# Kernel optimization log

Hardware: AMD Instinct MI355X
Metric: run time of the kernel (lower is better)

Reference implementation:

```python
import jax, jax.numpy as jnp
import numpy as np
import math

D_MODEL = 1024
NUM_HEADS = 16
HEAD_DIM = D_MODEL // NUM_HEADS


def setup_inputs() -> dict:
    key = jax.random.key(0)
    ks = jax.random.split(key, 9)
    B, S = 2, 2048
    scale = 1.0 / math.sqrt(D_MODEL)
    x = jax.random.normal(ks[0], (B, S, D_MODEL), dtype=jnp.float32)
    # torch nn.Linear params: weight [out, in], bias [out]
    Wq = jax.random.normal(ks[1], (D_MODEL, D_MODEL), dtype=jnp.float32) * scale
    bq = jax.random.normal(ks[2], (D_MODEL,), dtype=jnp.float32) * scale
    Wk = jax.random.normal(ks[3], (D_MODEL, D_MODEL), dtype=jnp.float32) * scale
    bk = jax.random.normal(ks[4], (D_MODEL,), dtype=jnp.float32) * scale
    Wv = jax.random.normal(ks[5], (D_MODEL, D_MODEL), dtype=jnp.float32) * scale
    bv = jax.random.normal(ks[6], (D_MODEL,), dtype=jnp.float32) * scale
    Wo = jax.random.normal(ks[7], (D_MODEL, D_MODEL), dtype=jnp.float32) * scale
    bo = jax.random.normal(ks[8], (D_MODEL,), dtype=jnp.float32) * scale
    return {"x": x, "Wq": Wq, "bq": bq, "Wk": Wk, "bk": bk,
            "Wv": Wv, "bv": bv, "Wo": Wo, "bo": bo}


def reference(x, Wq, bq, Wk, bk, Wv, bv, Wo, bo):
    B, S, _ = x.shape
    H, Dh = NUM_HEADS, HEAD_DIM

    def proj(W, b):
        # torch Linear: x @ W.T + b -> [B,S,D] -> [B,H,S,Dh]
        y = jnp.einsum('bsd,ed->bse', x, W) + b
        return y.reshape(B, S, H, Dh).transpose(0, 2, 1, 3)

    Q = proj(Wq, bq)
    K = proj(Wk, bk)
    V = proj(Wv, bv)

    # scores [B,H,S,S], causal mask with -inf, then scale by 1/sqrt(head_dim)
    scores = jnp.einsum('bhqd,bhkd->bhqk', Q, K)
    causal = jnp.tril(jnp.ones((S, S), dtype=bool))
    scores = jnp.where(causal, scores, -jnp.inf)
    A = jax.nn.softmax(scores / math.sqrt(Dh), axis=-1)

    O = jnp.einsum('bhqk,bhkd->bhqd', A, V)  # [B,H,S,Dh]
    O = O.transpose(0, 2, 1, 3).reshape(B, S, H * Dh)
    return jnp.einsum('bsd,ed->bse', O, Wo) + bo
```

## Files before the change

### kernel.cpp

```cpp
#include <hip/hip_runtime.h>


typedef _Float16 f16x8 __attribute__((ext_vector_type(8)));
typedef _Float16 f16x4 __attribute__((ext_vector_type(4)));
typedef _Float16 f16x2 __attribute__((ext_vector_type(2)));
typedef float f32x4 __attribute__((ext_vector_type(4)));

#define S_  2048
#define DM  1024
#define NH  16
#define DH  64

__device__ __forceinline__ void gload_lds16(const void* g, void* s) {
  __builtin_amdgcn_global_load_lds(
      (const __attribute__((address_space(1))) void*)g,
      (__attribute__((address_space(3))) void*)s, 16, 0, 0);
}

__device__ __forceinline__ f16x2 pkrtz(float a, float b) {
  return __builtin_bit_cast(f16x2, __builtin_amdgcn_cvt_pkrtz(a, b));
}


__global__ void cvt_all_kernel(const float* __restrict__ x,
                               const float* __restrict__ w0,
                               const float* __restrict__ w1,
                               const float* __restrict__ w2,
                               const float* __restrict__ w3,
                               _Float16* __restrict__ xb,
                               _Float16* __restrict__ wb) {
  const int bid = blockIdx.x;
  const float* src;
  _Float16* dst;
  int idx;
  if (bid < 4096) {
    src = x; dst = xb; idx = bid * 256 + threadIdx.x;
  } else {
    const int j = bid - 4096;
    const int y = j >> 10;
    src = (y == 0) ? w0 : (y == 1) ? w1 : (y == 2) ? w2 : w3;
    dst = wb + (size_t)y * (DM * DM);
    idx = (j & 1023) * 256 + threadIdx.x;
  }
  const float4 v = ((const float4*)src)[idx];
  f16x4 h;
  h[0] = (_Float16)v.x; h[1] = (_Float16)v.y;
  h[2] = (_Float16)v.z; h[3] = (_Float16)v.w;
  ((f16x4*)dst)[idx] = h;
}


__global__ __launch_bounds__(256, 3) void gemm_qkv_kernel(
    const _Float16* __restrict__ xb, const _Float16* __restrict__ wb,
    const float* __restrict__ bq, const float* __restrict__ bk,
    const float* __restrict__ bv, _Float16* __restrict__ qkv)
{
  __shared__ _Float16 As[2][128 * 32];
  __shared__ _Float16 Ws[2][128 * 32];

  const int i = blockIdx.x;
  const int xcd = i & 7;
  const int tt = i >> 3;
  const int mp = xcd * 4 + (tt & 3);
  const int u = tt >> 2;
  const int np = u & 7;
  const int z = u >> 3;

  const _Float16* W = wb + (size_t)z * (DM * DM);
  const float* bias = (z == 0) ? bq : ((z == 1) ? bk : bv);
  _Float16* out = qkv + (size_t)z * 4194304;

  const f32x4 z4 = {0.f, 0.f, 0.f, 0.f};
  f32x4 acc[4][4];
#pragma unroll
  for (int mi = 0; mi < 4; ++mi)
#pragma unroll
    for (int ni = 0; ni < 4; ++ni) acc[mi][ni] = z4;

  const int m0 = mp * 128, n0 = np * 128;
  const int t = threadIdx.x;
  const int w = t >> 6, l = t & 63;
  const int quad = l >> 4, ln = l & 15;
  const int wm = (w >> 1) << 6, wn = (w & 1) << 6;
  const int srow = l >> 2, scol = (l & 3) << 3;

  for (int k0 = 0; k0 < DM; k0 += 64) {
#pragma unroll
    for (int h = 0; h < 2; ++h)
#pragma unroll
      for (int i2 = 0; i2 < 2; ++i2) {
        const int ra = w * 32 + i2 * 16;
        gload_lds16(&xb[(size_t)(m0 + ra + srow) * DM + k0 + h * 32 + scol],
                    &As[h][ra * 32]);
        gload_lds16(&W[(size_t)(n0 + ra + srow) * DM + k0 + h * 32 + scol],
                    &Ws[h][ra * 32]);
      }
    __syncthreads();

#pragma unroll
    for (int h = 0; h < 2; ++h) {
      f16x8 af[4], bf[4];
#pragma unroll
      for (int mi = 0; mi < 4; ++mi)
        af[mi] = *(const f16x8*)&As[h][(wm + mi * 16 + ln) * 32 + quad * 8];
#pragma unroll
      for (int ni = 0; ni < 4; ++ni)
        bf[ni] = *(const f16x8*)&Ws[h][(wn + ni * 16 + ln) * 32 + quad * 8];
#pragma unroll
      for (int mi = 0; mi < 4; ++mi)
#pragma unroll
        for (int ni = 0; ni < 4; ++ni)
          acc[mi][ni] = __builtin_amdgcn_mfma_f32_16x16x32_f16(
              af[mi], bf[ni], acc[mi][ni], 0, 0, 0);
    }
    __syncthreads();
  }

  const float scale = (z == 0) ? 0.18033688f : 1.0f;

#pragma unroll
  for (int ni = 0; ni < 4; ++ni) {
    const int c = n0 + wn + ni * 16 + ln;
    const float bias_c = bias[c];
    const int h = c >> 6, d = c & 63;
#pragma unroll
    for (int mi = 0; mi < 4; ++mi) {
      const int mb = m0 + wm + mi * 16 + quad * 4;
#pragma unroll
      for (int r = 0; r < 4; ++r) {
        const int mg = mb + r;
        const int b = mg >> 11, s = mg & 2047;
        const int bh = b * NH + h;
        const float v = (acc[mi][ni][r] + bias_c) * scale;
        size_t idx;
        if (z == 2)
          idx = (size_t)bh * 131072 + (s >> 5) * 2048 + (d >> 4) * 512 +
                ((s >> 3) & 3) * 128 + (d & 15) * 8 + (s & 7);
        else
          idx = (size_t)bh * 131072 + (s >> 4) * 1024 + (d >> 5) * 512 +
                ((d >> 3) & 3) * 128 + (s & 15) * 8 + (d & 7);
        out[idx] = (_Float16)v;
      }
    }
  }
}


__global__ __launch_bounds__(256, 2) void gemm_out_kernel(
    const _Float16* __restrict__ ob, const _Float16* __restrict__ wo,
    const float* __restrict__ bo, float* __restrict__ out)
{
  __shared__ _Float16 As[2][128 * 32];
  __shared__ _Float16 Ws[2][64 * 32];

  const int i = blockIdx.x;
  const int xcd = i & 7;
  const int tt = i >> 3;
  const int mp = xcd * 4 + (tt & 3);
  const int np = tt >> 2;

  const f32x4 z4 = {0.f, 0.f, 0.f, 0.f};
  f32x4 acc[2][4];
#pragma unroll
  for (int mi = 0; mi < 2; ++mi)
#pragma unroll
    for (int ni = 0; ni < 4; ++ni) acc[mi][ni] = z4;

  const int m0 = mp * 128, n0 = np * 64;
  const int t = threadIdx.x;
  const int w = t >> 6, l = t & 63;
  const int quad = l >> 4, ln = l & 15;
  const int srow = l >> 2, scol = (l & 3) << 3;

  for (int k0 = 0; k0 < DM; k0 += 64) {
#pragma unroll
    for (int h = 0; h < 2; ++h) {
#pragma unroll
      for (int i2 = 0; i2 < 2; ++i2) {
        const int ra = w * 32 + i2 * 16;
        gload_lds16(&ob[(size_t)(m0 + ra + srow) * DM + k0 + h * 32 + scol],
                    &As[h][ra * 32]);
      }
      gload_lds16(&wo[(size_t)(n0 + w * 16 + srow) * DM + k0 + h * 32 + scol],
                  &Ws[h][w * 16 * 32]);
    }
    __syncthreads();

#pragma unroll
    for (int h = 0; h < 2; ++h) {
      f16x8 af[2], bf[4];
#pragma unroll
      for (int mi = 0; mi < 2; ++mi)
        af[mi] = *(const f16x8*)&As[h][(w * 32 + mi * 16 + ln) * 32 + quad * 8];
#pragma unroll
      for (int ni = 0; ni < 4; ++ni)
        bf[ni] = *(const f16x8*)&Ws[h][(ni * 16 + ln) * 32 + quad * 8];
#pragma unroll
      for (int mi = 0; mi < 2; ++mi)
#pragma unroll
        for (int ni = 0; ni < 4; ++ni)
          acc[mi][ni] = __builtin_amdgcn_mfma_f32_16x16x32_f16(
              af[mi], bf[ni], acc[mi][ni], 0, 0, 0);
    }
    __syncthreads();
  }

#pragma unroll
  for (int ni = 0; ni < 4; ++ni) {
    const int c = n0 + ni * 16 + ln;
    const float bias_c = bo[c];
#pragma unroll
    for (int mi = 0; mi < 2; ++mi) {
      const int mb = m0 + w * 32 + mi * 16 + quad * 4;
#pragma unroll
      for (int r = 0; r < 4; ++r)
        out[(size_t)(mb + r) * DM + c] = acc[mi][ni][r] + bias_c;
    }
  }
}


template <int MODE>
__device__ __forceinline__ void tile64(
    const _Float16* __restrict__ kb_, const _Float16* __restrict__ vb_,
    int t, const f16x8 (&qf)[4][2], f32x4 (&oacc)[4][4], float (&l_i)[4],
    _Float16* Ps, int quad, int ln, int l)
{
  f16x8 kr[4], vr[4];
#pragma unroll
  for (int ii = 0; ii < 4; ++ii)
    kr[ii] = *(const f16x8*)(kb_ + (size_t)t * 2048 + ii * 512 + l * 8);
#pragma unroll
  for (int ii = 0; ii < 4; ++ii)
    vr[ii] = *(const f16x8*)(vb_ + (size_t)t * 2048 + ii * 512 + l * 8);

  const f32x4 z4 = {0.f, 0.f, 0.f, 0.f};
#pragma unroll
  for (int qs = 0; qs < 4; ++qs) {
    if (MODE == 2 && qs < 2) continue;

    f32x4 sacc[2];
    sacc[0] = z4; sacc[1] = z4;
#pragma unroll
    for (int ks = 0; ks < 2; ++ks)
#pragma unroll
      for (int mi = 0; mi < 2; ++mi)
        sacc[mi] = __builtin_amdgcn_mfma_f32_16x16x32_f16(
            kr[mi * 2 + ks], qf[qs][ks], sacc[mi], 0, 0, 0);

    const bool DG = (MODE == 1 && qs < 2) || (MODE == 2);
    const int hq = ((MODE == 1) ? qs : (qs - 2)) << 4;

    float rs = 0.f;
#pragma unroll
    for (int mi = 0; mi < 2; ++mi) {
      float p[4];
#pragma unroll
      for (int r = 0; r < 4; ++r) {
        p[r] = __builtin_amdgcn_exp2f(sacc[mi][r]);
        if (DG && (mi * 16 + quad * 4 + r > hq + ln)) p[r] = 0.f;
        rs += p[r];
      }
      const f16x2 lo = pkrtz(p[0], p[1]);
      const f16x2 hi = pkrtz(p[2], p[3]);
      const f16x4 pk = __builtin_shufflevector(lo, hi, 0, 1, 2, 3);
      const int slot = ((mi * 4 + quad) + 2 * ln) & 15;
      *(f16x4*)&Ps[ln * 64 + slot * 4] = pk;
    }
    l_i[qs] += rs;

    const int slot2 = ((quad * 2) + 2 * ln) & 15;
    const f16x8 pb = *(const f16x8*)&Ps[ln * 64 + slot2 * 4];

#pragma unroll
    for (int di = 0; di < 4; ++di)
      oacc[qs][di] = __builtin_amdgcn_mfma_f32_16x16x32_f16(
          vr[di], pb, oacc[qs][di], 0, 0, 0);
  }
}

__global__ __launch_bounds__(128, 3) void attn_kernel(
    const _Float16* __restrict__ QF, const _Float16* __restrict__ KF,
    const _Float16* __restrict__ VF, _Float16* __restrict__ Ob)
{
  __shared__ _Float16 Ps[2][1024];
  __shared__ float mrgO[4][1024];
  __shared__ float mrgL[4][64];

  const int i = blockIdx.x;
  const int bh = i & 31;
  const int qb = 31 - (i >> 5);

  const int tid = threadIdx.x;
  const int e = tid >> 6, l = tid & 63;
  const int quad = l >> 4, ln = l & 15;

  const _Float16* qb_ = QF + (size_t)bh * 131072;
  const _Float16* kb_ = KF + (size_t)bh * 131072;
  const _Float16* vb_ = VF + (size_t)bh * 131072;
  _Float16* psw = &Ps[e][0];
  const int bidx = bh >> 4, hh = bh & 15;

  f16x8 qf[4][2];
#pragma unroll
  for (int qs = 0; qs < 4; ++qs)
#pragma unroll
    for (int ks = 0; ks < 2; ++ks)
      qf[qs][ks] = *(const f16x8*)
          (qb_ + (size_t)((4 * qb + qs) * 2 + ks) * 512 + l * 8);

  const f32x4 z4 = {0.f, 0.f, 0.f, 0.f};
  f32x4 oacc[4][4];
#pragma unroll
  for (int qs = 0; qs < 4; ++qs)
#pragma unroll
    for (int di = 0; di < 4; ++di) oacc[qs][di] = z4;
  float l_i[4] = {0.f, 0.f, 0.f, 0.f};

  int t = e;
  for (; t < 2 * qb; t += 2)
    tile64<0>(kb_, vb_, t, qf, oacc, l_i, psw, quad, ln, l);
  if (e == 0)
    tile64<1>(kb_, vb_, 2 * qb, qf, oacc, l_i, psw, quad, ln, l);
  else
    tile64<2>(kb_, vb_, 2 * qb + 1, qf, oacc, l_i, psw, quad, ln, l);

  if (e) {
#pragma unroll
    for (int qs = 0; qs < 4; ++qs) {
#pragma unroll
      for (int di = 0; di < 4; ++di)
        *(f32x4*)&mrgO[qs][di * 256 + l * 4] = oacc[qs][di];
      mrgL[qs][l] = l_i[qs];
    }
  }
  __syncthreads();
  if (!e) {
#pragma unroll
    for (int qs = 0; qs < 4; ++qs) {
#pragma unroll
      for (int di = 0; di < 4; ++di)
        oacc[qs][di] += *(const f32x4*)&mrgO[qs][di * 256 + l * 4];
      float li = l_i[qs] + mrgL[qs][l];
      li += __shfl_xor(li, 16);
      li += __shfl_xor(li, 32);
      const float inv = 1.0f / li;

      const int q = qb * 64 + qs * 16 + ln;
      _Float16* orow = Ob + (size_t)(bidx * S_ + q) * DM + hh * DH + quad * 4;
#pragma unroll
      for (int di = 0; di < 4; ++di) {
        f16x4 o4;
#pragma unroll
        for (int r = 0; r < 4; ++r)
          o4[r] = (_Float16)(oacc[qs][di][r] * inv);
        *(f16x4*)(orow + di * 16) = o4;
      }
    }
  }
}


extern "C" void kernel_launch(void* const* d_in, const int* in_sizes, int n_in,
                              void* d_out, int out_size, void* d_ws, size_t ws_size,
                              hipStream_t stream) {
  (void)in_sizes; (void)n_in; (void)out_size; (void)ws_size;
  const float* x  = (const float*)d_in[0];
  const float* Wq = (const float*)d_in[1];
  const float* bq = (const float*)d_in[2];
  const float* Wk = (const float*)d_in[3];
  const float* bk = (const float*)d_in[4];
  const float* Wv = (const float*)d_in[5];
  const float* bv = (const float*)d_in[6];
  const float* Wo = (const float*)d_in[7];
  const float* bo = (const float*)d_in[8];

  char* ws = (char*)d_ws;
  _Float16* xb  = (_Float16*)(ws);
  _Float16* wb  = (_Float16*)(ws + (8u << 20));
  _Float16* qkv = (_Float16*)(ws + (16u << 20));
  _Float16* ob  = (_Float16*)(ws + (40u << 20));

  cvt_all_kernel<<<dim3(8192), dim3(256), 0, stream>>>(x, Wq, Wk, Wv, Wo, xb, wb);
  gemm_qkv_kernel<<<dim3(768), dim3(256), 0, stream>>>(xb, wb, bq, bk, bv, qkv);
  attn_kernel<<<dim3(1024), dim3(128), 0, stream>>>(
      qkv, qkv + 4194304, qkv + 2 * 4194304, ob);
  gemm_out_kernel<<<dim3(512), dim3(256), 0, stream>>>(
      ob, wb + (size_t)3 * DM * DM, bo, (float*)d_out);
}
```

Measured before the change: 180.2 us.

## Split attention KV tiles across four waves with two-level tree merge

The attention kernel now uses 256 threads (4 waves) per block instead of 128, with each wave taking every fourth 64-wide KV tile rather than every second. Partial outputs and row sums are combined in two LDS reduction stages, pairs first and then the two survivors. The aim is more parallelism per query block, shortening the serial KV loop and reducing load imbalance from causal masking. The cost is extra LDS (doubled merge buffers), more barriers, and duplicated Q fragment loads per wave, which may lower occupancy.

```diff
diff --git a/kernel.cpp b/kernel.cpp
--- a/kernel.cpp
+++ b/kernel.cpp
@@ -279,13 +279,13 @@
   }
 }
 
-__global__ __launch_bounds__(128, 3) void attn_kernel(
+__global__ __launch_bounds__(256, 3) void attn_kernel(
     const _Float16* __restrict__ QF, const _Float16* __restrict__ KF,
     const _Float16* __restrict__ VF, _Float16* __restrict__ Ob)
 {
-  __shared__ _Float16 Ps[2][1024];
-  __shared__ float mrgO[4][1024];
-  __shared__ float mrgL[4][64];
+  __shared__ _Float16 Ps[4][1024];
+  __shared__ float mrgO[2][4][1024];
+  __shared__ float mrgL[2][4][64];
 
   const int i = blockIdx.x;
   const int bh = i & 31;
@@ -317,31 +317,52 @@
     for (int di = 0; di < 4; ++di) oacc[qs][di] = z4;
   float l_i[4] = {0.f, 0.f, 0.f, 0.f};
 
-  int t = e;
-  for (; t < 2 * qb; t += 2)
+  for (int t = e; t < 2 * qb; t += 4)
     tile64<0>(kb_, vb_, t, qf, oacc, l_i, psw, quad, ln, l);
-  if (e == 0)
+  if (((2 * qb) & 3) == e)
     tile64<1>(kb_, vb_, 2 * qb, qf, oacc, l_i, psw, quad, ln, l);
-  else
+  if (((2 * qb + 1) & 3) == e)
     tile64<2>(kb_, vb_, 2 * qb + 1, qf, oacc, l_i, psw, quad, ln, l);
 
-  if (e) {
+  if (e & 1) {
+    const int buf = e >> 1;
 #pragma unroll
     for (int qs = 0; qs < 4; ++qs) {
 #pragma unroll
       for (int di = 0; di < 4; ++di)
-        *(f32x4*)&mrgO[qs][di * 256 + l * 4] = oacc[qs][di];
-      mrgL[qs][l] = l_i[qs];
+        *(f32x4*)&mrgO[buf][qs][di * 256 + l * 4] = oacc[qs][di];
+      mrgL[buf][qs][l] = l_i[qs];
     }
   }
   __syncthreads();
-  if (!e) {
+  if (!(e & 1)) {
+    const int buf = e >> 1;
 #pragma unroll
     for (int qs = 0; qs < 4; ++qs) {
 #pragma unroll
       for (int di = 0; di < 4; ++di)
-        oacc[qs][di] += *(const f32x4*)&mrgO[qs][di * 256 + l * 4];
-      float li = l_i[qs] + mrgL[qs][l];
+        oacc[qs][di] += *(const f32x4*)&mrgO[buf][qs][di * 256 + l * 4];
+      l_i[qs] += mrgL[buf][qs][l];
+    }
+  }
+  __syncthreads();
+  if (e == 2) {
+#pragma unroll
+    for (int qs = 0; qs < 4; ++qs) {
+#pragma unroll
+      for (int di = 0; di < 4; ++di)
+        *(f32x4*)&mrgO[0][qs][di * 256 + l * 4] = oacc[qs][di];
+      mrgL[0][qs][l] = l_i[qs];
+    }
+  }
+  __syncthreads();
+  if (e == 0) {
+#pragma unroll
+    for (int qs = 0; qs < 4; ++qs) {
+#pragma unroll
+      for (int di = 0; di < 4; ++di)
+        oacc[qs][di] += *(const f32x4*)&mrgO[0][qs][di * 256 + l * 4];
+      float li = l_i[qs] + mrgL[0][qs][l];
       li += __shfl_xor(li, 16);
       li += __shfl_xor(li, 32);
       const float inv = 1.0f / li;
@@ -383,7 +404,7 @@
 
   cvt_all_kernel<<<dim3(8192), dim3(256), 0, stream>>>(x, Wq, Wk, Wv, Wo, xb, wb);
   gemm_qkv_kernel<<<dim3(768), dim3(256), 0, stream>>>(xb, wb, bq, bk, bv, qkv);
-  attn_kernel<<<dim3(1024), dim3(128), 0, stream>>>(
+  attn_kernel<<<dim3(1024), dim3(256), 0, stream>>>(
       qkv, qkv + 4194304, qkv + 2 * 4194304, ob);
   gemm_out_kernel<<<dim3(512), dim3(256), 0, stream>>>(
       ob, wb + (size_t)3 * DM * DM, bo, (float*)d_out);
```

Result: faster. 172.5 us (-4.2%).
